# Optimization experiments

Hardware: AMD Instinct MI355X
Metric: run time of the kernel (lower is better)

The kernel has to match this reference:

```python
import jax, jax.numpy as jnp
import numpy as np
from jax import lax

B = 32768   # batch_size
M = 14      # letters per word
H, WD = 16, 8  # input_dim -> cout_numel = 128 (SAME padding, stride 1)
L = 26      # num_labels
KS = 5      # conv kernel size (conv_layers[0][-1])
F = H * WD


def setup_inputs() -> dict:
    key = jax.random.key(0)
    k1, k2, k3, k4, k5 = jax.random.split(key, 5)
    X = jax.random.normal(k1, (B, M, F), dtype=jnp.float32)
    K = jax.random.normal(k2, (1, 1, KS, KS), dtype=jnp.float32) * 0.1  # conv kernel (OIHW)
    b = jax.random.normal(k3, (1,), dtype=jnp.float32) * 0.1            # conv bias
    W = jax.random.normal(k4, (L, F), dtype=jnp.float32)                # emission weights
    T = jax.random.normal(k5, (L, L), dtype=jnp.float32)                # transition matrix
    return {"X": X, "K": K, "b": b, "W": W, "T": T}


def _conv_features(X, K, b):
    # each letter image is a (1,H,W) map; SAME conv keeps spatial dims -> F features
    words = X.reshape(B * M, 1, H, WD)
    out = lax.conv_general_dilated(
        words, K, window_strides=(1, 1), padding="SAME",
        dimension_numbers=("NCHW", "OIHW", "NCHW")) + b
    return out.reshape(B, M, F)


def _viterbi(score, T):
    # score: (M, L) emission scores for one word; Viterbi max-decode
    def step(v, s):  # v: (L,) best path value ending at each label
        tot = v[:, None] + T          # (prev L, next L)
        bp = jnp.argmax(tot, axis=0)  # best previous label per next label
        v_new = jnp.max(tot, axis=0) + s
        return v_new, bp

    v_last, bps = lax.scan(step, score[0], score[1:])  # bps: (M-1, L)
    last = jnp.argmax(v_last)

    def back(nxt, bp):
        cur = bp[nxt]
        return cur, cur

    _, idxs = lax.scan(back, last, bps, reverse=True)  # (M-1,)
    path = jnp.concatenate([idxs, last[None]])         # (M,)
    return path.astype(jnp.int32)


def reference(X, K, b, W, T):
    feats = _conv_features(X, K, b)                 # (B, M, F)
    scores = jnp.einsum("bmf,lf->bml", feats, W)    # (B, M, L) emission scores
    decods = jax.vmap(lambda s: _viterbi(s, T))(scores)  # (B, M)
    return decods[..., None]                        # (B, M, 1) int32, matches torch output
```

## Files before the change

kernel.cpp:

```cpp
#include <hip/hip_runtime.h>
#include <math.h>

#define LBL 26
#define MM  14
#define FF  128
#define HH  16
#define WW  8
#define KSZ 5
#define WPB 16
#define LPB (WPB * MM)
#define NITER 8

__global__ void prep_kernel(const float* __restrict__ K,
                            const float* __restrict__ b,
                            const float* __restrict__ W,
                            float* __restrict__ w2,
                            float* __restrict__ cvec) {
    int idx = blockIdx.x * blockDim.x + threadIdx.x;
    int stride = gridDim.x * blockDim.x;
    for (int o = idx; o < LBL * FF; o += stride) {
        int l = o / FF, f = o % FF;
        int qy = f / WW, qx = f % WW;
        double acc = 0.0;
        for (int ky = 0; ky < KSZ; ++ky) {
            int y = qy - ky + 2;
            if (y < 0 || y >= HH) continue;
            for (int kx = 0; kx < KSZ; ++kx) {
                int x = qx - kx + 2;
                if (x < 0 || x >= WW) continue;
                acc += (double)K[ky * KSZ + kx] * (double)W[l * FF + y * WW + x];
            }
        }
        w2[o] = (float)acc;
    }
    for (int l = idx; l < LBL; l += stride) {
        double s = 0.0;
        for (int f = 0; f < FF; ++f) s += (double)W[l * FF + f];
        cvec[l] = (float)(s * (double)b[0]);
    }
}

template <int PAD>
__global__ __launch_bounds__(256) void scores_kernel(const float* __restrict__ X,
                                                     const float* __restrict__ w2,
                                                     const float* __restrict__ cvec,
                                                     float* __restrict__ sV) {
    __shared__ float4 wtile[32][LBL];
    __shared__ float  slds[256 * LBL];

    const int tid    = threadIdx.x;
    const int letter = blockIdx.x * 256 + tid;

    const float4* W4 = (const float4*)w2;
    for (int i = tid; i < 32 * LBL; i += 256) {
        const int l = i >> 5, q = i & 31;
        wtile[q][l] = W4[i];
    }
    __syncthreads();

    const float4* xr = (const float4*)X + (size_t)letter * 32;

    float acc[LBL];
#pragma unroll
    for (int l = 0; l < LBL; ++l) acc[l] = cvec[l];

#define COMPUTE(g, C0, C1, C2, C3)                                         \
    {                                                                      \
        _Pragma("unroll")                                                  \
        for (int l = 0; l < LBL; ++l) {                                    \
            const float4 w0 = wtile[4 * (g) + 0][l];        \
            const float4 w1 = wtile[4 * (g) + 1][l];                       \
            const float4 w2v = wtile[4 * (g) + 2][l];                      \
            const float4 w3 = wtile[4 * (g) + 3][l];                       \
            float a = acc[l];                                              \
            a = fmaf(C0.x, w0.x, a); a = fmaf(C0.y, w0.y, a);              \
            a = fmaf(C0.z, w0.z, a); a = fmaf(C0.w, w0.w, a);              \
            a = fmaf(C1.x, w1.x, a); a = fmaf(C1.y, w1.y, a);              \
            a = fmaf(C1.z, w1.z, a); a = fmaf(C1.w, w1.w, a);              \
            a = fmaf(C2.x, w2v.x, a); a = fmaf(C2.y, w2v.y, a);            \
            a = fmaf(C2.z, w2v.z, a); a = fmaf(C2.w, w2v.w, a);            \
            a = fmaf(C3.x, w3.x, a); a = fmaf(C3.y, w3.y, a);              \
            a = fmaf(C3.z, w3.z, a); a = fmaf(C3.w, w3.w, a);              \
            acc[l] = a;                                                    \
        }                                                                  \
    }

    float4 c0 = xr[0], c1 = xr[1], c2 = xr[2], c3 = xr[3];
    for (int g = 0; g < 7; ++g) {
        const float4 n0 = xr[4 * g + 4], n1 = xr[4 * g + 5];
        const float4 n2 = xr[4 * g + 6], n3 = xr[4 * g + 7];
        COMPUTE(g, c0, c1, c2, c3)
        c0 = n0; c1 = n1; c2 = n2; c3 = n3;
    }
    COMPUTE(7, c0, c1, c2, c3)
#undef COMPUTE

#pragma unroll
    for (int l = 0; l < LBL; ++l) slds[tid * LBL + l] = acc[l];
    __syncthreads();
    const size_t obase = (size_t)blockIdx.x * 256 * PAD;
    for (int idx = tid; idx < 256 * PAD; idx += 256) {
        const int ll = idx / PAD, lw = idx - ll * PAD;
        sV[obase + idx] = (lw < LBL) ? slds[ll * LBL + lw] : 0.0f;
    }
}

template <int PAD>
__global__ __launch_bounds__(256) void viterbi_kernel(const float* __restrict__ sV,
                                                      const float* __restrict__ Tm,
                                                      int* __restrict__ out) {
    __shared__ float T_lds[LBL * LBL];
    __shared__ float vb[8][32];

    const int tid  = threadIdx.x;
    for (int i = tid; i < LBL * LBL; i += 256) T_lds[i] = Tm[i];
    __syncthreads();

    const int wv   = tid >> 6;
    const int lane = tid & 63;
    const int half = lane >> 5;
    const int j    = lane & 31;
    const int jc   = (j < LBL) ? j : 25;

    const int wl   = wv * 2 + half;
    const int word = blockIdx.x * 8 + wl;
    const float* sw = sV + (size_t)word * (MM * PAD);

    float tcol[LBL];
#pragma unroll
    for (int i = 0; i < LBL; ++i) tcol[i] = T_lds[i * LBL + jc];

    float* vbw = &vb[wl][0];
    float v = (j < LBL) ? sw[j] : -INFINITY;
    vbw[j] = v;
    unsigned bp_pack[4] = {0u, 0u, 0u, 0u};

#pragma unroll
    for (int t = 1; t < MM; ++t) {
        const float se = sw[t * PAD + jc];
        float best = -INFINITY;
        int bi = 0;
        const float4* q4 = (const float4*)vbw;
#define VCHK(vexpr, idx) { const float val = (vexpr) + tcol[idx]; \
                           if (val > best) { best = val; bi = idx; } }
        {
            float4 qq;
            qq = q4[0]; VCHK(qq.x, 0) VCHK(qq.y, 1) VCHK(qq.z, 2) VCHK(qq.w, 3)
            qq = q4[1]; VCHK(qq.x, 4) VCHK(qq.y, 5) VCHK(qq.z, 6) VCHK(qq.w, 7)
            qq = q4[2]; VCHK(qq.x, 8) VCHK(qq.y, 9) VCHK(qq.z, 10) VCHK(qq.w, 11)
            qq = q4[3]; VCHK(qq.x, 12) VCHK(qq.y, 13) VCHK(qq.z, 14) VCHK(qq.w, 15)
            qq = q4[4]; VCHK(qq.x, 16) VCHK(qq.y, 17) VCHK(qq.z, 18) VCHK(qq.w, 19)
            qq = q4[5]; VCHK(qq.x, 20) VCHK(qq.y, 21) VCHK(qq.z, 22) VCHK(qq.w, 23)
            qq = q4[6]; VCHK(qq.x, 24) VCHK(qq.y, 25)
        }
#undef VCHK
        v = (j < LBL) ? (best + se) : -INFINITY;
        vbw[j] = v;
        const int k = t - 1;
        bp_pack[k >> 2] |= (unsigned)bi << ((k & 3) * 8);
    }

    float best = v;
    int bidx = (j < LBL) ? j : 999;
#pragma unroll
    for (int d = 1; d < 32; d <<= 1) {
        const float ov = __shfl_xor(best, d, 64);
        const int oi = __shfl_xor(bidx, d, 64);
        if (ov > best || (ov == best && oi < bidx)) { best = ov; bidx = oi; }
    }

    int cur = bidx;
    if (j == 0) out[word * MM + (MM - 1)] = cur;
#pragma unroll
    for (int k = MM - 2; k >= 0; --k) {
        const unsigned packed = __shfl(bp_pack[k >> 2], (lane & 32) | cur, 64);
        cur = (int)((packed >> ((k & 3) * 8)) & 0xffu);
        if (j == 0) out[word * MM + k] = cur;
    }
}

__global__ __launch_bounds__(256) void crf_kernel(const float* __restrict__ X,
                                                  const float* __restrict__ T,
                                                  const float* __restrict__ w2,
                                                  const float* __restrict__ cvec,
                                                  int* __restrict__ out) {
    __shared__ float4 tile[LPB * 4];
    __shared__ float  s_lds[WPB * MM * LBL];
    __shared__ float  v_lds[WPB * 32];

    const int tid = threadIdx.x;
    const int blk = blockIdx.x;
    const float4* X4 = (const float4*)X + (size_t)blk * LPB * (FF / 4);
    const float4* W4 = (const float4*)w2;

    float acc[LBL];
    if (tid < LPB) {
#pragma unroll
        for (int l = 0; l < LBL; ++l) acc[l] = cvec[l];
    }
    const int c0 = tid, c1 = tid + 256, c2 = tid + 512, c3 = tid + 768;
    float4 st0, st1, st2, st3;
    st0 = X4[(c0 >> 2) * 32 + (c0 & 3)];
    st1 = X4[(c1 >> 2) * 32 + (c1 & 3)];
    st2 = X4[(c2 >> 2) * 32 + (c2 & 3)];
    if (tid < 128) st3 = X4[(c3 >> 2) * 32 + (c3 & 3)];

    for (int iter = 0; iter < NITER; ++iter) {
        tile[(c0 >> 2) * 4 + ((c0 & 3) ^ ((c0 >> 2) & 3))] = st0;
        tile[(c1 >> 2) * 4 + ((c1 & 3) ^ ((c1 >> 2) & 3))] = st1;
        tile[(c2 >> 2) * 4 + ((c2 & 3) ^ ((c2 >> 2) & 3))] = st2;
        if (tid < 128) tile[(c3 >> 2) * 4 + ((c3 & 3) ^ ((c3 >> 2) & 3))] = st3;
        __syncthreads();
        if (iter + 1 < NITER) {
            const int ofs = (iter + 1) * 4;
            st0 = X4[(c0 >> 2) * 32 + ofs + (c0 & 3)];
            st1 = X4[(c1 >> 2) * 32 + ofs + (c1 & 3)];
            st2 = X4[(c2 >> 2) * 32 + ofs + (c2 & 3)];
            if (tid < 128) st3 = X4[(c3 >> 2) * 32 + ofs + (c3 & 3)];
        }
        if (tid < LPB) {
            const float4 xv0 = tile[tid * 4 + (0 ^ (tid & 3))];
            const float4 xv1 = tile[tid * 4 + (1 ^ (tid & 3))];
            const float4 xv2 = tile[tid * 4 + (2 ^ (tid & 3))];
            const float4 xv3 = tile[tid * 4 + (3 ^ (tid & 3))];
#pragma unroll
            for (int l = 0; l < LBL; ++l) {
                const float4 w0 = W4[l * 32 + iter * 4 + 0];
                const float4 w1 = W4[l * 32 + iter * 4 + 1];
                const float4 w2v = W4[l * 32 + iter * 4 + 2];
                const float4 w3 = W4[l * 32 + iter * 4 + 3];
                float a = acc[l];
                a = fmaf(xv0.x, w0.x, a); a = fmaf(xv0.y, w0.y, a);
                a = fmaf(xv0.z, w0.z, a); a = fmaf(xv0.w, w0.w, a);
                a = fmaf(xv1.x, w1.x, a); a = fmaf(xv1.y, w1.y, a);
                a = fmaf(xv1.z, w1.z, a); a = fmaf(xv1.w, w1.w, a);
                a = fmaf(xv2.x, w2v.x, a); a = fmaf(xv2.y, w2v.y, a);
                a = fmaf(xv2.z, w2v.z, a); a = fmaf(xv2.w, w2v.w, a);
                a = fmaf(xv3.x, w3.x, a); a = fmaf(xv3.y, w3.y, a);
                a = fmaf(xv3.z, w3.z, a); a = fmaf(xv3.w, w3.w, a);
                acc[l] = a;
            }
        }
        __syncthreads();
    }
    if (tid < LPB) {
#pragma unroll
        for (int l = 0; l < LBL; ++l) s_lds[tid * LBL + l] = acc[l];
    }
    __syncthreads();

    const int lane = tid & 63;
    const int wvid = tid >> 6;
    const int half = lane >> 5;
    const int j = lane & 31;
    const int jc = (j < LBL) ? j : 0;

    float tcol[LBL];
#pragma unroll
    for (int i = 0; i < LBL; ++i) tcol[i] = T[i * LBL + jc];

    for (int pass = 0; pass < 2; ++pass) {
        const int wi = pass * 8 + wvid * 2 + half;
        const int word = blk * WPB + wi;
        const float* sw = s_lds + wi * MM * LBL;
        float* vbp = v_lds + wi * 32;

        float v = (j < LBL) ? sw[j] : -INFINITY;
        if (j < LBL) vbp[j] = v;
        unsigned bp_pack[4] = {0u, 0u, 0u, 0u};

#pragma unroll
        for (int t = 1; t < MM; ++t) {
            float best = -INFINITY;
            int bi = 0;
#define VCHK(vexpr, idx) { const float val = (vexpr) + tcol[idx]; \
                           if (val > best) { best = val; bi = idx; } }
            {
                float4 vv;
                vv = *(const float4*)(vbp + 0);
                VCHK(vv.x, 0) VCHK(vv.y, 1) VCHK(vv.z, 2) VCHK(vv.w, 3)
                vv = *(const float4*)(vbp + 4);
                VCHK(vv.x, 4) VCHK(vv.y, 5) VCHK(vv.z, 6) VCHK(vv.w, 7)
                vv = *(const float4*)(vbp + 8);
                VCHK(vv.x, 8) VCHK(vv.y, 9) VCHK(vv.z, 10) VCHK(vv.w, 11)
                vv = *(const float4*)(vbp + 12);
                VCHK(vv.x, 12) VCHK(vv.y, 13) VCHK(vv.z, 14) VCHK(vv.w, 15)
                vv = *(const float4*)(vbp + 16);
                VCHK(vv.x, 16) VCHK(vv.y, 17) VCHK(vv.z, 18) VCHK(vv.w, 19)
                vv = *(const float4*)(vbp + 20);
                VCHK(vv.x, 20) VCHK(vv.y, 21) VCHK(vv.z, 22) VCHK(vv.w, 23)
                vv = *(const float4*)(vbp + 24);
                VCHK(vv.x, 24) VCHK(vv.y, 25)
            }
#undef VCHK
            v = (j < LBL) ? (best + sw[t * LBL + j]) : -INFINITY;
            if (j < LBL) vbp[j] = v;
            const int k = t - 1;
            bp_pack[k >> 2] |= (unsigned)bi << ((k & 3) * 8);
        }

        float best = v;
        int bidx = (j < LBL) ? j : 999;
#pragma unroll
        for (int d = 1; d < 32; d <<= 1) {
            const float ov = __shfl_xor(best, d, 64);
            const int oi = __shfl_xor(bidx, d, 64);
            if (ov > best || (ov == best && oi < bidx)) { best = ov; bidx = oi; }
        }
        int cur = bidx;
        if (j == 0) out[word * MM + (MM - 1)] = cur;
#pragma unroll
        for (int k = MM - 2; k >= 0; --k) {
            const unsigned packed = __shfl(bp_pack[k >> 2], (lane & 32) | cur, 64);
            cur = (int)((packed >> ((k & 3) * 8)) & 0xffu);
            if (j == 0) out[word * MM + k] = cur;
        }
        __syncthreads();
    }
}

extern "C" void kernel_launch(void* const* d_in, const int* in_sizes, int n_in,
                              void* d_out, int out_size, void* d_ws, size_t ws_size,
                              hipStream_t stream) {
    const float* X = (const float*)d_in[0];
    const float* K = (const float*)d_in[1];
    const float* b = (const float*)d_in[2];
    const float* W = (const float*)d_in[3];
    const float* T = (const float*)d_in[4];
    int* out = (int*)d_out;

    const int nw = in_sizes[0] / (MM * FF);
    const int NLET = nw * MM;

    const size_t w_bytes = (size_t)(LBL * FF + LBL) * sizeof(float);
    const size_t sV28    = (size_t)NLET * 28 * sizeof(float);
    const size_t sV26    = (size_t)NLET * 26 * sizeof(float);

    const bool shape_ok = (NLET % 256) == 0 && (nw % 8) == 0;

    if (shape_ok && ws_size >= sV28 + w_bytes) {
        float* sV   = (float*)d_ws;
        float* w2   = (float*)((char*)d_ws + sV28);
        float* cvec = w2 + LBL * FF;
        prep_kernel<<<(LBL * FF + 255) / 256, 256, 0, stream>>>(K, b, W, w2, cvec);
        scores_kernel<28><<<NLET / 256, 256, 0, stream>>>(X, w2, cvec, sV);
        viterbi_kernel<28><<<nw / 8, 256, 0, stream>>>(sV, T, out);
    } else if (shape_ok && ws_size >= sV26 + w_bytes) {
        float* sV   = (float*)d_ws;
        float* w2   = (float*)((char*)d_ws + sV26);
        float* cvec = w2 + LBL * FF;
        prep_kernel<<<(LBL * FF + 255) / 256, 256, 0, stream>>>(K, b, W, w2, cvec);
        scores_kernel<26><<<NLET / 256, 256, 0, stream>>>(X, w2, cvec, sV);
        viterbi_kernel<26><<<nw / 8, 256, 0, stream>>>(sV, T, out);
    } else {
        float* w2   = (float*)d_ws;
        float* cvec = w2 + LBL * FF;
        prep_kernel<<<(LBL * FF + 255) / 256, 256, 0, stream>>>(K, b, W, w2, cvec);
        crf_kernel<<<nw / WPB, 256, 0, stream>>>(X, T, w2, cvec, out);
    }
}
```

Baseline: 146.2 us.

## Fuse emission scoring and Viterbi decode into one kernel via LDS

Adds a fused kernel that computes per-letter emission scores with an LDS-resident weight tile, writes them into a padded shared buffer, and runs Viterbi decoding for 16 words per block in the same launch. This drops the global score buffer round-trip and one kernel launch. It also removes the old crf fallback and the PAD=26 path. The cost is that only 224 of 256 threads do the dot-product phase, and the shared-memory footprint is larger, which may lower occupancy.

```diff
diff --git a/kernel.cpp b/kernel.cpp
--- a/kernel.cpp
+++ b/kernel.cpp
@@ -9,7 +9,7 @@
 #define KSZ 5
 #define WPB 16
 #define LPB (WPB * MM)
-#define NITER 8
+#define SST 29
 
 __global__ void prep_kernel(const float* __restrict__ K,
                             const float* __restrict__ b,
@@ -40,16 +40,17 @@
     }
 }
 
-template <int PAD>
-__global__ __launch_bounds__(256) void scores_kernel(const float* __restrict__ X,
-                                                     const float* __restrict__ w2,
-                                                     const float* __restrict__ cvec,
-                                                     float* __restrict__ sV) {
+__global__ __launch_bounds__(256) void fused_kernel(const float* __restrict__ X,
+                                                    const float* __restrict__ w2,
+                                                    const float* __restrict__ cvec,
+                                                    const float* __restrict__ Tm,
+                                                    int* __restrict__ out) {
     __shared__ float4 wtile[32][LBL];
-    __shared__ float  slds[256 * LBL];
-
-    const int tid    = threadIdx.x;
-    const int letter = blockIdx.x * 256 + tid;
+    __shared__ float  s_lds[WPB][MM][SST];
+    __shared__ float  vb[8][32];
+
+    const int tid = threadIdx.x;
+    const int blk = blockIdx.x;
 
     const float4* W4 = (const float4*)w2;
     for (int i = tid; i < 32 * LBL; i += 256) {
@@ -58,11 +59,13 @@
     }
     __syncthreads();
 
-    const float4* xr = (const float4*)X + (size_t)letter * 32;
-
-    float acc[LBL];
-#pragma unroll
-    for (int l = 0; l < LBL; ++l) acc[l] = cvec[l];
+    if (tid < LPB) {
+        const int letter = blk * LPB + tid;
+        const float4* xr = (const float4*)X + (size_t)letter * 32;
+
+        float acc[LBL];
+#pragma unroll
+        for (int l = 0; l < LBL; ++l) acc[l] = cvec[l];
 
 #define COMPUTE(g, C0, C1, C2, C3)                                         \
     {                                                                      \
@@ -85,6 +88,135 @@
         }                                                                  \
     }
 
+        float4 c0 = xr[0], c1 = xr[1], c2 = xr[2], c3 = xr[3];
+        for (int g = 0; g < 7; ++g) {
+            const float4 n0 = xr[4 * g + 4], n1 = xr[4 * g + 5];
+            const float4 n2 = xr[4 * g + 6], n3 = xr[4 * g + 7];
+            COMPUTE(g, c0, c1, c2, c3)
+            c0 = n0; c1 = n1; c2 = n2; c3 = n3;
+        }
+        COMPUTE(7, c0, c1, c2, c3)
+#undef COMPUTE
+
+        float* dst = &s_lds[0][0][0] + tid * SST;
+#pragma unroll
+        for (int l = 0; l < LBL; ++l) dst[l] = acc[l];
+    }
+    __syncthreads();
+
+    const int wv   = tid >> 6;
+    const int lane = tid & 63;
+    const int half = lane >> 5;
+    const int j    = lane & 31;
+    const int jc   = (j < LBL) ? j : 25;
+
+    const int wl = wv * 2 + half;
+
+    float tcol[LBL];
+#pragma unroll
+    for (int i = 0; i < LBL; ++i) tcol[i] = Tm[i * LBL + jc];
+
+    float* vbw = &vb[wl][0];
+
+    for (int pass = 0; pass < 2; ++pass) {
+        const int lwl  = pass * 8 + wl;
+        const int word = blk * WPB + lwl;
+        const float* sw = &s_lds[lwl][0][0];
+
+        float v = (j < LBL) ? sw[j] : -INFINITY;
+        vbw[j] = v;
+        unsigned bp_pack[4] = {0u, 0u, 0u, 0u};
+
+#pragma unroll
+        for (int t = 1; t < MM; ++t) {
+            const float se = sw[t * SST + jc];
+            float best = -INFINITY;
+            int bi = 0;
+            const float4* q4 = (const float4*)vbw;
+#define VCHK(vexpr, idx) { const float val = (vexpr) + tcol[idx]; \
+                           if (val > best) { best = val; bi = idx; } }
+            {
+                float4 qq;
+                qq = q4[0]; VCHK(qq.x, 0) VCHK(qq.y, 1) VCHK(qq.z, 2) VCHK(qq.w, 3)
+                qq = q4[1]; VCHK(qq.x, 4) VCHK(qq.y, 5) VCHK(qq.z, 6) VCHK(qq.w, 7)
+                qq = q4[2]; VCHK(qq.x, 8) VCHK(qq.y, 9) VCHK(qq.z, 10) VCHK(qq.w, 11)
+                qq = q4[3]; VCHK(qq.x, 12) VCHK(qq.y, 13) VCHK(qq.z, 14) VCHK(qq.w, 15)
+                qq = q4[4]; VCHK(qq.x, 16) VCHK(qq.y, 17) VCHK(qq.z, 18) VCHK(qq.w, 19)
+                qq = q4[5]; VCHK(qq.x, 20) VCHK(qq.y, 21) VCHK(qq.z, 22) VCHK(qq.w, 23)
+                qq = q4[6]; VCHK(qq.x, 24) VCHK(qq.y, 25)
+            }
+#undef VCHK
+            v = (j < LBL) ? (best + se) : -INFINITY;
+            vbw[j] = v;
+            const int k = t - 1;
+            bp_pack[k >> 2] |= (unsigned)bi << ((k & 3) * 8);
+        }
+
+        float best = v;
+        int bidx = (j < LBL) ? j : 999;
+#pragma unroll
+        for (int d = 1; d < 32; d <<= 1) {
+            const float ov = __shfl_xor(best, d, 64);
+            const int oi = __shfl_xor(bidx, d, 64);
+            if (ov > best || (ov == best && oi < bidx)) { best = ov; bidx = oi; }
+        }
+
+        int cur = bidx;
+        if (j == 0) out[word * MM + (MM - 1)] = cur;
+#pragma unroll
+        for (int k = MM - 2; k >= 0; --k) {
+            const unsigned packed = __shfl(bp_pack[k >> 2], (lane & 32) | cur, 64);
+            cur = (int)((packed >> ((k & 3) * 8)) & 0xffu);
+            if (j == 0) out[word * MM + k] = cur;
+        }
+    }
+}
+
+template <int PAD>
+__global__ __launch_bounds__(256) void scores_kernel(const float* __restrict__ X,
+                                                     const float* __restrict__ w2,
+                                                     const float* __restrict__ cvec,
+                                                     float* __restrict__ sV) {
+    __shared__ float4 wtile[32][LBL];
+    __shared__ float  slds[256 * LBL];
+
+    const int tid    = threadIdx.x;
+    const int letter = blockIdx.x * 256 + tid;
+
+    const float4* W4 = (const float4*)w2;
+    for (int i = tid; i < 32 * LBL; i += 256) {
+        const int l = i >> 5, q = i & 31;
+        wtile[q][l] = W4[i];
+    }
+    __syncthreads();
+
+    const float4* xr = (const float4*)X + (size_t)letter * 32;
+
+    float acc[LBL];
+#pragma unroll
+    for (int l = 0; l < LBL; ++l) acc[l] = cvec[l];
+
+#define COMPUTE(g, C0, C1, C2, C3)                                         \
+    {                                                                      \
+        _Pragma("unroll")                                                  \
+        for (int l = 0; l < LBL; ++l) {                                    \
+            const float4 w0 = wtile[4 * (g) + 0][l];                       \
+            const float4 w1 = wtile[4 * (g) + 1][l];                       \
+            const float4 w2v = wtile[4 * (g) + 2][l];                      \
+            const float4 w3 = wtile[4 * (g) + 3][l];                       \
+            float a = acc[l];                                              \
+            a = fmaf(C0.x, w0.x, a); a = fmaf(C0.y, w0.y, a);              \
+            a = fmaf(C0.z, w0.z, a); a = fmaf(C0.w, w0.w, a);              \
+            a = fmaf(C1.x, w1.x, a); a = fmaf(C1.y, w1.y, a);              \
+            a = fmaf(C1.z, w1.z, a); a = fmaf(C1.w, w1.w, a);              \
+            a = fmaf(C2.x, w2v.x, a); a = fmaf(C2.y, w2v.y, a);            \
+            a = fmaf(C2.z, w2v.z, a); a = fmaf(C2.w, w2v.w, a);            \
+            a = fmaf(C3.x, w3.x, a); a = fmaf(C3.y, w3.y, a);              \
+            a = fmaf(C3.z, w3.z, a); a = fmaf(C3.w, w3.w, a);              \
+            acc[l] = a;                                                    \
+        }                                                                  \
+    }
+
     float4 c0 = xr[0], c1 = xr[1], c2 = xr[2], c3 = xr[3];
     for (int g = 0; g < 7; ++g) {
         const float4 n0 = xr[4 * g + 4], n1 = xr[4 * g + 5];
@@ -179,146 +311,6 @@
     }
 }
 
-__global__ __launch_bounds__(256) void crf_kernel(const float* __restrict__ X,
-                                                  const float* __restrict__ T,
-                                                  const float* __restrict__ w2,
-                                                  const float* __restrict__ cvec,
-                                                  int* __restrict__ out) {
-    __shared__ float4 tile[LPB * 4];
-    __shared__ float  s_lds[WPB * MM * LBL];
-    __shared__ float  v_lds[WPB * 32];
-
-    const int tid = threadIdx.x;
-    const int blk = blockIdx.x;
-    const float4* X4 = (const float4*)X + (size_t)blk * LPB * (FF / 4);
-    const float4* W4 = (const float4*)w2;
-
-    float acc[LBL];
-    if (tid < LPB) {
-#pragma unroll
-        for (int l = 0; l < LBL; ++l) acc[l] = cvec[l];
-    }
-    const int c0 = tid, c1 = tid + 256, c2 = tid + 512, c3 = tid + 768;
-    float4 st0, st1, st2, st3;
-    st0 = X4[(c0 >> 2) * 32 + (c0 & 3)];
-    st1 = X4[(c1 >> 2) * 32 + (c1 & 3)];
-    st2 = X4[(c2 >> 2) * 32 + (c2 & 3)];
-    if (tid < 128) st3 = X4[(c3 >> 2) * 32 + (c3 & 3)];
-
-    for (int iter = 0; iter < NITER; ++iter) {
-        tile[(c0 >> 2) * 4 + ((c0 & 3) ^ ((c0 >> 2) & 3))] = st0;
-        tile[(c1 >> 2) * 4 + ((c1 & 3) ^ ((c1 >> 2) & 3))] = st1;
-        tile[(c2 >> 2) * 4 + ((c2 & 3) ^ ((c2 >> 2) & 3))] = st2;
-        if (tid < 128) tile[(c3 >> 2) * 4 + ((c3 & 3) ^ ((c3 >> 2) & 3))] = st3;
-        __syncthreads();
-        if (iter + 1 < NITER) {
-            const int ofs = (iter + 1) * 4;
-            st0 = X4[(c0 >> 2) * 32 + ofs + (c0 & 3)];
-            st1 = X4[(c1 >> 2) * 32 + ofs + (c1 & 3)];
-            st2 = X4[(c2 >> 2) * 32 + ofs + (c2 & 3)];
-            if (tid < 128) st3 = X4[(c3 >> 2) * 32 + ofs + (c3 & 3)];
-        }
-        if (tid < LPB) {
-            const float4 xv0 = tile[tid * 4 + (0 ^ (tid & 3))];
-            const float4 xv1 = tile[tid * 4 + (1 ^ (tid & 3))];
-            const float4 xv2 = tile[tid * 4 + (2 ^ (tid & 3))];
-            const float4 xv3 = tile[tid * 4 + (3 ^ (tid & 3))];
-#pragma unroll
-            for (int l = 0; l < LBL; ++l) {
-                const float4 w0 = W4[l * 32 + iter * 4 + 0];
-                const float4 w1 = W4[l * 32 + iter * 4 + 1];
-                const float4 w2v = W4[l * 32 + iter * 4 + 2];
-                const float4 w3 = W4[l * 32 + iter * 4 + 3];
-                float a = acc[l];
-                a = fmaf(xv0.x, w0.x, a); a = fmaf(xv0.y, w0.y, a);
-                a = fmaf(xv0.z, w0.z, a); a = fmaf(xv0.w, w0.w, a);
-                a = fmaf(xv1.x, w1.x, a); a = fmaf(xv1.y, w1.y, a);
-                a = fmaf(xv1.z, w1.z, a); a = fmaf(xv1.w, w1.w, a);
-                a = fmaf(xv2.x, w2v.x, a); a = fmaf(xv2.y, w2v.y, a);
-                a = fmaf(xv2.z, w2v.z, a); a = fmaf(xv2.w, w2v.w, a);
-                a = fmaf(xv3.x, w3.x, a); a = fmaf(xv3.y, w3.y, a);
-                a = fmaf(xv3.z, w3.z, a); a = fmaf(xv3.w, w3.w, a);
-                acc[l] = a;
-            }
-        }
-        __syncthreads();
-    }
-    if (tid < LPB) {
-#pragma unroll
-        for (int l = 0; l < LBL; ++l) s_lds[tid * LBL + l] = acc[l];
-    }
-    __syncthreads();
-
-    const int lane = tid & 63;
-    const int wvid = tid >> 6;
-    const int half = lane >> 5;
-    const int j = lane & 31;
-    const int jc = (j < LBL) ? j : 0;
-
-    float tcol[LBL];
-#pragma unroll
-    for (int i = 0; i < LBL; ++i) tcol[i] = T[i * LBL + jc];
-
-    for (int pass = 0; pass < 2; ++pass) {
-        const int wi = pass * 8 + wvid * 2 + half;
-        const int word = blk * WPB + wi;
-        const float* sw = s_lds + wi * MM * LBL;
-        float* vbp = v_lds + wi * 32;
-
-        float v = (j < LBL) ? sw[j] : -INFINITY;
-        if (j < LBL) vbp[j] = v;
-        unsigned bp_pack[4] = {0u, 0u, 0u, 0u};
-
-#pragma unroll
-        for (int t = 1; t < MM; ++t) {
-            float best = -INFINITY;
-            int bi = 0;
-#define VCHK(vexpr, idx) { const float val = (vexpr) + tcol[idx]; \
-                           if (val > best) { best = val; bi = idx; } }
-            {
-                float4 vv;
-                vv = *(const float4*)(vbp + 0);
-                VCHK(vv.x, 0) VCHK(vv.y, 1) VCHK(vv.z, 2) VCHK(vv.w, 3)
-                vv = *(const float4*)(vbp + 4);
-                VCHK(vv.x, 4) VCHK(vv.y, 5) VCHK(vv.z, 6) VCHK(vv.w, 7)
-                vv = *(const float4*)(vbp + 8);
-                VCHK(vv.x, 8) VCHK(vv.y, 9) VCHK(vv.z, 10) VCHK(vv.w, 11)
-                vv = *(const float4*)(vbp + 12);
-                VCHK(vv.x, 12) VCHK(vv.y, 13) VCHK(vv.z, 14) VCHK(vv.w, 15)
-                vv = *(const float4*)(vbp + 16);
-                VCHK(vv.x, 16) VCHK(vv.y, 17) VCHK(vv.z, 18) VCHK(vv.w, 19)
-                vv = *(const float4*)(vbp + 20);
-                VCHK(vv.x, 20) VCHK(vv.y, 21) VCHK(vv.z, 22) VCHK(vv.w, 23)
-                vv = *(const float4*)(vbp + 24);
-                VCHK(vv.x, 24) VCHK(vv.y, 25)
-            }
-#undef VCHK
-            v = (j < LBL) ? (best + sw[t * LBL + j]) : -INFINITY;
-            if (j < LBL) vbp[j] = v;
-            const int k = t - 1;
-            bp_pack[k >> 2] |= (unsigned)bi << ((k & 3) * 8);
-        }
-
-        float best = v;
-        int bidx = (j < LBL) ? j : 999;
-#pragma unroll
-        for (int d = 1; d < 32; d <<= 1) {
-            const float ov = __shfl_xor(best, d, 64);
-            const int oi = __shfl_xor(bidx, d, 64);
-            if (ov > best || (ov == best && oi < bidx)) { best = ov; bidx = oi; }
-        }
-        int cur = bidx;
-        if (j == 0) out[word * MM + (MM - 1)] = cur;
-#pragma unroll
-        for (int k = MM - 2; k >= 0; --k) {
-            const unsigned packed = __shfl(bp_pack[k >> 2], (lane & 32) | cur, 64);
-            cur = (int)((packed >> ((k & 3) * 8)) & 0xffu);
-            if (j == 0) out[word * MM + k] = cur;
-        }
-        __syncthreads();
-    }
-}
-
 extern "C" void kernel_launch(void* const* d_in, const int* in_sizes, int n_in,
                               void* d_out, int out_size, void* d_ws, size_t ws_size,
                               hipStream_t stream) {
@@ -334,28 +326,18 @@
 
     const size_t w_bytes = (size_t)(LBL * FF + LBL) * sizeof(float);
     const size_t sV28    = (size_t)NLET * 28 * sizeof(float);
-    const size_t sV26    = (size_t)NLET * 26 * sizeof(float);
-
-    const bool shape_ok = (NLET % 256) == 0 && (nw % 8) == 0;
-
-    if (shape_ok && ws_size >= sV28 + w_bytes) {
+
+    if ((NLET % LPB) == 0 && (nw % WPB) == 0 && ws_size >= w_bytes) {
+        float* w2   = (float*)d_ws;
+        float* cvec = w2 + LBL * FF;
+        prep_kernel<<<(LBL * FF + 255) / 256, 256, 0, stream>>>(K, b, W, w2, cvec);
+        fused_kernel<<<NLET / LPB, 256, 0, stream>>>(X, w2, cvec, T, out);
+    } else if ((NLET % 256) == 0 && (nw % 8) == 0 && ws_size >= sV28 + w_bytes) {
         float* sV   = (float*)d_ws;
         float* w2   = (float*)((char*)d_ws + sV28);
         float* cvec = w2 + LBL * FF;
         prep_kernel<<<(LBL * FF + 255) / 256, 256, 0, stream>>>(K, b, W, w2, cvec);
         scores_kernel<28><<<NLET / 256, 256, 0, stream>>>(X, w2, cvec, sV);
         viterbi_kernel<28><<<nw / 8, 256, 0, stream>>>(sV, T, out);
-    } else if (shape_ok && ws_size >= sV26 + w_bytes) {
-        float* sV   = (float*)d_ws;
-        float* w2   = (float*)((char*)d_ws + sV26);
-        float* cvec = w2 + LBL * FF;
-        prep_kernel<<<(LBL * FF + 255) / 256, 256, 0, stream>>>(K, b, W, w2, cvec);
-        scores_kernel<26><<<NLET / 256, 256, 0, stream>>>(X, w2, cvec, sV);
-        viterbi_kernel<26><<<nw / 8, 256, 0, stream>>>(sV, T, out);
-    } else {
-        float* w2   = (float*)d_ws;
-        float* cvec = w2 + LBL * FF;
-        prep_kernel<<<(LBL * FF + 255) / 256, 256, 0, stream>>>(K, b, W, w2, cvec);
-        crf_kernel<<<nw / WPB, 256, 0, stream>>>(X, T, w2, cvec, out);
-    }
-}
+    }
+}
```

Measured after the change: 149.9 us. +2.6%, slower.
